# Kernel tuning notes

Measured on AMD Instinct MI355X. Metric: run time of the kernel, lower is better.

## Reference

```python
import jax, jax.numpy as jnp
import numpy as np

B, C, H, W = 4, 512, 48, 48
DQ = C // 8  # inter_rate = 8
N = H * W
EPS = 1e-5


def _local_mask(radius):
    r = np.arange(N) // W
    c = np.arange(N) % W
    d = np.maximum(np.abs(r[:, None] - r[None, :]), np.abs(c[:, None] - c[None, :]))
    return jnp.asarray(d <= radius)


def setup_inputs() -> dict:
    key = jax.random.key(0)
    ks = jax.random.split(key, 12)
    def nrm(k, shape, scale=0.04):
        return jax.random.normal(k, shape, dtype=jnp.float32) * scale
    zc = jnp.zeros((C,), jnp.float32)
    oc = jnp.ones((C,), jnp.float32)
    return {
        "x": jax.random.normal(ks[0], (B, C, H, W), dtype=jnp.float32),
        "Wq": nrm(ks[1], (DQ, C)), "bq": jnp.zeros((DQ,), jnp.float32),
        "Wk": nrm(ks[2], (DQ, C)), "bk": jnp.zeros((DQ,), jnp.float32),
        "Wv": nrm(ks[3], (C, C)), "bv": zc,
        "conv1_w": nrm(ks[4], (C, C, 3, 3)),
        "bn1_w": oc, "bn1_b": zc, "bn1_m": zc, "bn1_v": oc,
        "conv2_w": nrm(ks[5], (C, C, 3, 3)),
        "bn2_w": oc, "bn2_b": zc, "bn2_m": zc, "bn2_v": oc,
        "sig1_w": nrm(ks[6], (C, C)), "sig1_b": zc,
        "sig2_w": nrm(ks[7], (C, C)), "sig2_b": zc,
        "gamma": jnp.full((1,), 0.5, jnp.float32),
        "gamma1": jnp.full((1,), 0.3, jnp.float32),
        "gamma2": jnp.full((1,), 0.2, jnp.float32),
        "mask1": _local_mask(6),
        "mask2": _local_mask(12),
    }


def _masked_softmax(e, mask):
    # exp(e)*mask / sum(exp(e)*mask) == softmax with -inf outside mask
    e = e - jnp.max(e, axis=-1, keepdims=True)
    w = jnp.exp(e) * mask.astype(e.dtype)
    return w / jnp.sum(w, axis=-1, keepdims=True)


def _conv1x1(t, w, b):
    return jnp.einsum('bchw,dc->bdhw', t, w) + b[None, :, None, None]


def _conv3x3_bn_relu(t, w, g, beta, mu, var):
    y = jax.lax.conv_general_dilated(t, w, (1, 1), 'SAME',
                                     dimension_numbers=('NCHW', 'OIHW', 'NCHW'))
    scale = (g / jnp.sqrt(var + EPS))[None, :, None, None]
    y = (y - mu[None, :, None, None]) * scale + beta[None, :, None, None]
    return jax.nn.relu(y)


def _forward(x, Wq, bq, Wk, bk, Wv, bv, conv1_w, bn1_w, bn1_b, bn1_m, bn1_v,
             conv2_w, bn2_w, bn2_b, bn2_m, bn2_v, sig1_w, sig1_b, sig2_w, sig2_b,
             gamma, gamma1, gamma2, mask1, mask2):
    b, c, h, w = x.shape
    n = h * w
    q = _conv1x1(x, Wq, bq).reshape(b, -1, n)   # [B, d, N]
    k = _conv1x1(x, Wk, bk).reshape(b, -1, n)   # [B, d, N]
    energy = jnp.einsum('bdn,bdm->bnm', q, k)   # [B, N, N] (query rows)
    a0 = jax.nn.softmax(energy, axis=-1)
    a1 = _masked_softmax(energy, mask1)
    a2 = _masked_softmax(energy, mask2)
    v = _conv1x1(x, Wv, bv).reshape(b, c, n)
    # torch: bmm(value, attention.permute(0,2,1)) -> out[b,c,m] = sum_n v[b,c,n]*a[m,n]
    out0 = jnp.einsum('bcn,bmn->bcm', v, a0).reshape(b, c, h, w)
    out0 = gamma * out0 + x
    out0 = _conv3x3_bn_relu(out0, conv1_w, bn1_w, bn1_b, bn1_m, bn1_v)
    s1 = (jax.nn.sigmoid(_conv1x1(out0, sig1_w, sig1_b)) * out0).reshape(b, c, n)
    out1 = jnp.einsum('bcn,bmn->bcm', s1, a1).reshape(b, c, h, w)
    out1 = gamma1 * out1 + out0
    out1 = _conv3x3_bn_relu(out1, conv2_w, bn2_w, bn2_b, bn2_m, bn2_v)
    s2 = (jax.nn.sigmoid(_conv1x1(out1, sig2_w, sig2_b)) * out1).reshape(b, c, n)
    out2 = jnp.einsum('bcn,bmn->bcm', s2, a2).reshape(b, c, h, w)
    return gamma2 * out2 + out1


def reference(x, Wq, bq, Wk, bk, Wv, bv, conv1_w, bn1_w, bn1_b, bn1_m, bn1_v,
              conv2_w, bn2_w, bn2_b, bn2_m, bn2_v, sig1_w, sig1_b, sig2_w, sig2_b,
              gamma, gamma1, gamma2, mask1, mask2):
    return _forward(x, Wq, bq, Wk, bk, Wv, bv, conv1_w, bn1_w, bn1_b, bn1_m, bn1_v,
                    conv2_w, bn2_w, bn2_b, bn2_m, bn2_v, sig1_w, sig1_b, sig2_w, sig2_b,
                    gamma, gamma1, gamma2, mask1, mask2)
```

## Files before the change

kernel.cpp:

```cpp
#include <hip/hip_runtime.h>
#include <math.h>

#define BB 4
#define CC 512
#define HH 48
#define WW 48
#define NN 2304
#define DDQ 64
#define LDSP 72
#define PW 50
#define PROWS 2500

typedef __attribute__((ext_vector_type(4))) float f32x4;
typedef __attribute__((ext_vector_type(8))) _Float16 half8;
typedef __attribute__((ext_vector_type(4))) _Float16 half4;
typedef __attribute__((ext_vector_type(8))) short bf16x8;

__device__ __forceinline__ int imax(int a, int b) { return a > b ? a : b; }
__device__ __forceinline__ int imin(int a, int b) { return a < b ? a : b; }
__device__ __forceinline__ int prow(int m) {
    int h = m / WW, w = m - h * WW;
    return (h + 1) * PW + (w + 1);
}
__device__ __forceinline__ unsigned short f2bf(float f) {
    unsigned u = __float_as_uint(f);
    u += 0x7fffu + ((u >> 16) & 1u);
    return (unsigned short)(u >> 16);
}
__device__ __forceinline__ float bf2f(unsigned short s) {
    unsigned u = ((unsigned)s) << 16;
    return __uint_as_float(u);
}

typedef __attribute__((address_space(1))) unsigned int g_u32;
typedef __attribute__((address_space(3))) unsigned int l_u32;
__device__ __forceinline__ void gl16(const void* g, void* l) {
    __builtin_amdgcn_global_load_lds((const g_u32*)g, (l_u32*)l, 16, 0, 0);
}

#define BWAVE_IDX()                                  \
    int tid = threadIdx.x;                           \
    int wave = tid >> 6, lane = tid & 63;            \
    int wm = (wave >> 1) * 64, wn = (wave & 1) * 32; \
    int x = lane & 15, qq = lane >> 4;

__device__ __forceinline__ half8 fragld(const _Float16* T, int r, int c) {
    int kb = c ^ (r & 7);
    return *(const half8*)(T + r * 64 + kb * 8);
}
__device__ __forceinline__ bf16x8 fragld_b(const unsigned short* T, int r, int c) {
    int kb = c ^ (r & 7);
    return *(const bf16x8*)(T + r * 64 + kb * 8);
}

__device__ __forceinline__ void btile(const _Float16* As, const _Float16* Bs,
                                      f32x4 acc[4][2], int wm, int wn, int x, int qq) {
#pragma unroll
    for (int ks = 0; ks < 2; ++ks) {
        int c = ks * 4 + qq;
        half8 a0 = fragld(As, wm + x, c);
        half8 a1 = fragld(As, wm + 16 + x, c);
        half8 a2 = fragld(As, wm + 32 + x, c);
        half8 a3 = fragld(As, wm + 48 + x, c);
        half8 b0 = fragld(Bs, wn + x, c);
        half8 b1 = fragld(Bs, wn + 16 + x, c);
        acc[0][0] = __builtin_amdgcn_mfma_f32_16x16x32_f16(a0, b0, acc[0][0], 0, 0, 0);
        acc[0][1] = __builtin_amdgcn_mfma_f32_16x16x32_f16(a0, b1, acc[0][1], 0, 0, 0);
        acc[1][0] = __builtin_amdgcn_mfma_f32_16x16x32_f16(a1, b0, acc[1][0], 0, 0, 0);
        acc[1][1] = __builtin_amdgcn_mfma_f32_16x16x32_f16(a1, b1, acc[1][1], 0, 0, 0);
        acc[2][0] = __builtin_amdgcn_mfma_f32_16x16x32_f16(a2, b0, acc[2][0], 0, 0, 0);
        acc[2][1] = __builtin_amdgcn_mfma_f32_16x16x32_f16(a2, b1, acc[2][1], 0, 0, 0);
        acc[3][0] = __builtin_amdgcn_mfma_f32_16x16x32_f16(a3, b0, acc[3][0], 0, 0, 0);
        acc[3][1] = __builtin_amdgcn_mfma_f32_16x16x32_f16(a3, b1, acc[3][1], 0, 0, 0);
    }
}
__device__ __forceinline__ void btile_b(const unsigned short* As, const unsigned short* Bs,
                                        f32x4 acc[4][2], int wm, int wn, int x, int qq) {
#pragma unroll
    for (int ks = 0; ks < 2; ++ks) {
        int c = ks * 4 + qq;
        bf16x8 a0 = fragld_b(As, wm + x, c);
        bf16x8 a1 = fragld_b(As, wm + 16 + x, c);
        bf16x8 a2 = fragld_b(As, wm + 32 + x, c);
        bf16x8 a3 = fragld_b(As, wm + 48 + x, c);
        bf16x8 b0 = fragld_b(Bs, wn + x, c);
        bf16x8 b1 = fragld_b(Bs, wn + 16 + x, c);
        acc[0][0] = __builtin_amdgcn_mfma_f32_16x16x32_bf16(a0, b0, acc[0][0], 0, 0, 0);
        acc[0][1] = __builtin_amdgcn_mfma_f32_16x16x32_bf16(a0, b1, acc[0][1], 0, 0, 0);
        acc[1][0] = __builtin_amdgcn_mfma_f32_16x16x32_bf16(a1, b0, acc[1][0], 0, 0, 0);
        acc[1][1] = __builtin_amdgcn_mfma_f32_16x16x32_bf16(a1, b1, acc[1][1], 0, 0, 0);
        acc[2][0] = __builtin_amdgcn_mfma_f32_16x16x32_bf16(a2, b0, acc[2][0], 0, 0, 0);
        acc[2][1] = __builtin_amdgcn_mfma_f32_16x16x32_bf16(a2, b1, acc[2][1], 0, 0, 0);
        acc[3][0] = __builtin_amdgcn_mfma_f32_16x16x32_bf16(a3, b0, acc[3][0], 0, 0, 0);
        acc[3][1] = __builtin_amdgcn_mfma_f32_16x16x32_bf16(a3, b1, acc[3][1], 0, 0, 0);
    }
}

#define BACC_INIT()                                         \
    f32x4 zf = {0.f, 0.f, 0.f, 0.f};                        \
    f32x4 acc[4][2];                                        \
    _Pragma("unroll") for (int i_ = 0; i_ < 4; ++i_) {      \
        acc[i_][0] = zf; acc[i_][1] = zf; }

#define SLOT_A(i) int sb = (wave * 4 + (i)) * 64; int s = sb + lane; \
                  int r = s >> 3, kb = s & 7; int koff = ((kb ^ (r & 7)) << 3);
#define SLOT_B(i) int sb = (wave * 2 + (i)) * 64; int s = sb + lane; \
                  int r = s >> 3, kb = s & 7; int koff = ((kb ^ (r & 7)) << 3);

__device__ __forceinline__ void stage_rows(_Float16* dst, const _Float16* __restrict__ src,
                                           int ld, int row0, int k0, int tid) {
#pragma unroll
    for (int i = 0; i < 2; ++i) {
        int s = tid * 2 + i;
        int r = s >> 3, off = (s & 7) << 3;
        *(half8*)(dst + r * LDSP + off) =
            *(const half8*)(src + (size_t)(row0 + r) * ld + k0 + off);
    }
}
__device__ __forceinline__ void mfma_tile(const _Float16* As, const _Float16* Bs,
                                          f32x4 acc[2][2], int wm, int wn, int x, int qq) {
#pragma unroll
    for (int ks = 0; ks < 2; ++ks) {
        int kof = ks * 32 + qq * 8;
        half8 a0 = *(const half8*)(As + (wm + x) * LDSP + kof);
        half8 a1 = *(const half8*)(As + (wm + 16 + x) * LDSP + kof);
        half8 b0 = *(const half8*)(Bs + (wn + x) * LDSP + kof);
        half8 b1 = *(const half8*)(Bs + (wn + 16 + x) * LDSP + kof);
        acc[0][0] = __builtin_amdgcn_mfma_f32_16x16x32_f16(a0, b0, acc[0][0], 0, 0, 0);
        acc[0][1] = __builtin_amdgcn_mfma_f32_16x16x32_f16(a0, b1, acc[0][1], 0, 0, 0);
        acc[1][0] = __builtin_amdgcn_mfma_f32_16x16x32_f16(a1, b0, acc[1][0], 0, 0, 0);
        acc[1][1] = __builtin_amdgcn_mfma_f32_16x16x32_f16(a1, b1, acc[1][1], 0, 0, 0);
    }
}
#define WAVE_IDX()                             \
    int tid = threadIdx.x;                     \
    int wave = tid >> 6, lane = tid & 63;      \
    int wm = (wave >> 1) * 32, wn = (wave & 1) * 32; \
    int x = lane & 15, qq = lane >> 4;
#define ACC_INIT()                             \
    f32x4 zf = {0.f, 0.f, 0.f, 0.f};           \
    f32x4 acc[2][2];                           \
    acc[0][0] = zf; acc[0][1] = zf; acc[1][0] = zf; acc[1][1] = zf;

__global__ __launch_bounds__(256) void k_cast_multi(const float* __restrict__ s0,
                                                    const float* __restrict__ s1,
                                                    const float* __restrict__ s2,
                                                    _Float16* __restrict__ d0,
                                                    _Float16* __restrict__ d1,
                                                    _Float16* __restrict__ d2, int n) {
    const float* s = blockIdx.y == 0 ? s0 : (blockIdx.y == 1 ? s1 : s2);
    _Float16* d = blockIdx.y == 0 ? d0 : (blockIdx.y == 1 ? d1 : d2);
    for (int i = blockIdx.x * 256 + threadIdx.x; i < n; i += gridDim.x * 256)
        d[i] = (_Float16)s[i];
}

__global__ __launch_bounds__(256) void k_repack_conv2(const float* __restrict__ w1,
                                                      const float* __restrict__ w2,
                                                      _Float16* __restrict__ d1,
                                                      _Float16* __restrict__ d2) {
    const float* w = blockIdx.y ? w2 : w1;
    _Float16* dst = blockIdx.y ? d2 : d1;
    int i = blockIdx.x * 256 + threadIdx.x;
    if (i >= 9 * CC * CC) return;
    int r = i / (CC * CC);
    int rem = i - r * CC * CC;
    int co = rem / CC, ci = rem - (rem / CC) * CC;
    dst[i] = (_Float16)w[((size_t)co * CC + ci) * 9 + r];
}

__global__ __launch_bounds__(256) void k_transpose_x(const float* __restrict__ x,
                                                     _Float16* __restrict__ xT) {
    __shared__ float tile[32][33];
    int b = blockIdx.z;
    int c0 = blockIdx.y * 32, n0 = blockIdx.x * 32;
    int tx = threadIdx.x & 31, ty = threadIdx.x >> 5;
    const float* xb = x + (size_t)b * CC * NN;
#pragma unroll
    for (int rr = 0; rr < 32; rr += 8)
        tile[ty + rr][tx] = xb[(size_t)(c0 + ty + rr) * NN + n0 + tx];
    __syncthreads();
    _Float16* xTb = xT + (size_t)b * NN * CC;
#pragma unroll
    for (int rr = 0; rr < 32; rr += 8)
        xTb[(size_t)(n0 + ty + rr) * CC + c0 + tx] = (_Float16)tile[tx][ty + rr];
}

__global__ __launch_bounds__(256) void k_qkproj(const _Float16* __restrict__ Wq,
                                                const _Float16* __restrict__ Wk,
                                                const float* __restrict__ bq,
                                                const float* __restrict__ bk,
                                                const _Float16* __restrict__ xT,
                                                _Float16* __restrict__ qT,
                                                _Float16* __restrict__ kT) {
    __shared__ _Float16 As[64 * LDSP];
    __shared__ _Float16 Bs[64 * LDSP];
    WAVE_IDX();
    int j0 = blockIdx.x * 64, b = blockIdx.z;
    const _Float16* Wp = blockIdx.y ? Wk : Wq;
    const float* bias = blockIdx.y ? bk : bq;
    _Float16* outT = blockIdx.y ? kT : qT;
    const _Float16* xTb = xT + (size_t)b * NN * CC;
    ACC_INIT();
    for (int kc = 0; kc < CC; kc += 64) {
        stage_rows(As, Wp, CC, 0, kc, tid);
        stage_rows(Bs, xTb, CC, j0, kc, tid);
        __syncthreads();
        mfma_tile(As, Bs, acc, wm, wn, x, qq);
        __syncthreads();
    }
#pragma unroll
    for (int ms = 0; ms < 2; ++ms) {
        int R0 = wm + ms * 16 + qq * 4;
#pragma unroll
        for (int ns = 0; ns < 2; ++ns) {
            int Ccol = j0 + wn + ns * 16 + x;
            half4 t;
            t.x = (_Float16)(acc[ms][ns][0] + bias[R0 + 0]);
            t.y = (_Float16)(acc[ms][ns][1] + bias[R0 + 1]);
            t.z = (_Float16)(acc[ms][ns][2] + bias[R0 + 2]);
            t.w = (_Float16)(acc[ms][ns][3] + bias[R0 + 3]);
            *(half4*)(outT + ((size_t)b * NN + Ccol) * DDQ + R0) = t;
        }
    }
}

template <int EPI, int PAD>
__global__ __launch_bounds__(256) void k_cgemm(const _Float16* __restrict__ W,
                                               const float* __restrict__ bias,
                                               const _Float16* __restrict__ Bsrc,
                                               const float* __restrict__ gate,
                                               unsigned short* __restrict__ out) {
    __shared__ __align__(16) _Float16 As[2][128 * 64];
    __shared__ __align__(16) _Float16 Bs[2][64 * 64];
    BWAVE_IDX();
    int j0 = blockIdx.x * 64, i0 = blockIdx.y * 128, b = blockIdx.z;
    const _Float16* Bb = Bsrc + (size_t)b * (PAD ? (size_t)PROWS * CC : (size_t)NN * CC);

    const _Float16* aSrc[4]; int aOf[4];
#pragma unroll
    for (int i = 0; i < 4; ++i) {
        SLOT_A(i);
        aSrc[i] = W + (size_t)(i0 + r) * CC + koff;
        aOf[i] = sb * 8;
    }
    const _Float16* bSrc[2]; int bOf[2];
#pragma unroll
    for (int i = 0; i < 2; ++i) {
        SLOT_B(i);
        int row = PAD ? prow(j0 + r) : (j0 + r);
        bSrc[i] = Bb + (size_t)row * CC + koff;
        bOf[i] = sb * 8;
    }
    BACC_INIT();
#pragma unroll
    for (int i = 0; i < 4; ++i) gl16(aSrc[i], As[0] + aOf[i]);
#pragma unroll
    for (int i = 0; i < 2; ++i) gl16(bSrc[i], Bs[0] + bOf[i]);
    const int NSTEP = CC / 64;
#pragma unroll
    for (int t = 0; t < NSTEP - 1; ++t) {
        __syncthreads();
        int kc = (t + 1) << 6;
        int nb = (t + 1) & 1;
#pragma unroll
        for (int i = 0; i < 4; ++i) gl16(aSrc[i] + kc, As[nb] + aOf[i]);
#pragma unroll
        for (int i = 0; i < 2; ++i) gl16(bSrc[i] + kc, Bs[nb] + bOf[i]);
        btile(As[t & 1], Bs[t & 1], acc, wm, wn, x, qq);
    }
    __syncthreads();
    btile(As[(NSTEP - 1) & 1], Bs[(NSTEP - 1) & 1], acc, wm, wn, x, qq);
#pragma unroll
    for (int mt = 0; mt < 4; ++mt) {
        int R0 = i0 + wm + mt * 16 + qq * 4;
#pragma unroll
        for (int nt = 0; nt < 2; ++nt) {
            int Ccol = j0 + wn + nt * 16 + x;
#pragma unroll
            for (int e = 0; e < 4; ++e) {
                float v = acc[mt][nt][e] + bias[R0 + e];
                size_t idx = ((size_t)b * CC + R0 + e) * NN + Ccol;
                if (EPI == 1) v = gate[idx] / (1.f + __expf(-v));
                out[idx] = f2bf(v);
            }
        }
    }
}

__global__ __launch_bounds__(256) void k_exp(const _Float16* __restrict__ qT,
                                             const _Float16* __restrict__ kT,
                                             unsigned short* __restrict__ attnB,
                                             float* __restrict__ rowsum, int rad) {
    __shared__ _Float16 qs[64 * LDSP];
    __shared__ _Float16 ks[64 * LDSP];
    __shared__ unsigned short Eh[64 * 72];
    __shared__ float psum[512];
    WAVE_IDX();
    int j0 = blockIdx.x * 64, i0 = blockIdx.y * 64, b = blockIdx.z;
    if (rad > 0) {
        int hlo = i0 / WW, hhi = (i0 + 63) / WW;
        int h2lo = imax(0, hlo - rad), h2hi = imin(HH - 1, hhi + rad);
        int klo = (h2lo * WW) & ~63;
        int khi = imin(NN, ((h2hi + 1) * WW + 63) & ~63);
        if (j0 + 64 <= klo || j0 >= khi) return;
    }
    stage_rows(qs, qT + (size_t)b * NN * DDQ, DDQ, i0, 0, tid);
    stage_rows(ks, kT + (size_t)b * NN * DDQ, DDQ, j0, 0, tid);
    __syncthreads();
    ACC_INIT();
    mfma_tile(qs, ks, acc, wm, wn, x, qq);
#pragma unroll
    for (int ns = 0; ns < 2; ++ns) {
        int col = wn + ns * 16 + x;
        int gn = j0 + col;
        int hn = gn / WW, cn = gn % WW;
#pragma unroll
        for (int ms = 0; ms < 2; ++ms)
#pragma unroll
            for (int e = 0; e < 4; ++e) {
                int row = wm + ms * 16 + qq * 4 + e;
                int gm = i0 + row;
                bool valid = true;
                if (rad > 0) {
                    int dh = gm / WW - hn; if (dh < 0) dh = -dh;
                    int dc = gm % WW - cn; if (dc < 0) dc = -dc;
                    valid = (dh <= rad) && (dc <= rad);
                }
                float w = valid ? __expf(acc[ms][ns][e]) : 0.f;
                Eh[row * 72 + col] = f2bf(w);
            }
    }
    __syncthreads();
#pragma unroll
    for (int t = 0; t < 2; ++t) {
        int s = tid + t * 256;
        int r = s >> 3, cg = (s & 7) << 3;
        bf16x8 v = *(const bf16x8*)(Eh + r * 72 + cg);
        *(bf16x8*)(attnB + ((size_t)b * NN + i0 + r) * NN + j0 + cg) = v;
        float ss = 0.f;
#pragma unroll
        for (int j = 0; j < 8; ++j) ss += bf2f((unsigned short)v[j]);
        psum[s] = ss;
    }
    __syncthreads();
    if (tid < 64) {
        float tot = 0.f;
#pragma unroll
        for (int g = 0; g < 8; ++g) tot += psum[tid * 8 + g];
        atomicAdd(rowsum + (size_t)b * NN + i0 + tid, tot);
    }
}

__global__ __launch_bounds__(256) void k_attn(const unsigned short* __restrict__ A,
                                              const unsigned short* __restrict__ attnB,
                                              const float* __restrict__ rowsum,
                                              const float* __restrict__ res,
                                              const float* __restrict__ gamma,
                                              float* __restrict__ outF,
                                              _Float16* __restrict__ outT, int rad) {
    __shared__ __align__(16) unsigned short As[2][128 * 64];
    __shared__ __align__(16) unsigned short Bs[2][64 * 64];
    BWAVE_IDX();
    int j0 = blockIdx.x * 64, i0 = blockIdx.y * 128, b = blockIdx.z;
    int klo = 0, khi = NN;
    if (rad > 0) {
        int hlo = j0 / WW, hhi = (j0 + 63) / WW;
        int h2lo = imax(0, hlo - rad), h2hi = imin(HH - 1, hhi + rad);
        klo = (h2lo * WW) & ~63;
        khi = imin(NN, ((h2hi + 1) * WW + 63) & ~63);
    }
    const unsigned short* Ab = A + (size_t)b * CC * NN;
    const unsigned short* Tb = attnB + (size_t)b * NN * NN;

    const unsigned short* aSrc[4]; int aOf[4];
#pragma unroll
    for (int i = 0; i < 4; ++i) {
        SLOT_A(i);
        aSrc[i] = Ab + (size_t)(i0 + r) * NN + koff + klo;
        aOf[i] = sb * 8;
    }
    const unsigned short* bSrc[2]; int bOf[2];
#pragma unroll
    for (int i = 0; i < 2; ++i) {
        SLOT_B(i);
        bSrc[i] = Tb + (size_t)(j0 + r) * NN + koff + klo;
        bOf[i] = sb * 8;
    }
    BACC_INIT();
    int nsteps = (khi - klo) >> 6;
#pragma unroll
    for (int i = 0; i < 4; ++i) gl16(aSrc[i], As[0] + aOf[i]);
#pragma unroll
    for (int i = 0; i < 2; ++i) gl16(bSrc[i], Bs[0] + bOf[i]);
    for (int t = 0; t < nsteps - 1; ++t) {
        __syncthreads();
        int kc = (t + 1) << 6;
        int nb = (t + 1) & 1;
#pragma unroll
        for (int i = 0; i < 4; ++i) gl16(aSrc[i] + kc, As[nb] + aOf[i]);
#pragma unroll
        for (int i = 0; i < 2; ++i) gl16(bSrc[i] + kc, Bs[nb] + bOf[i]);
        btile_b(As[t & 1], Bs[t & 1], acc, wm, wn, x, qq);
    }
    __syncthreads();
    btile_b(As[(nsteps - 1) & 1], Bs[(nsteps - 1) & 1], acc, wm, wn, x, qq);
    float g = gamma[0];
#pragma unroll
    for (int mt = 0; mt < 4; ++mt) {
        int R0 = i0 + wm + mt * 16 + qq * 4;
#pragma unroll
        for (int nt = 0; nt < 2; ++nt) {
            int Ccol = j0 + wn + nt * 16 + x;
            float linv = g / fmaxf(rowsum[(size_t)b * NN + Ccol], 1e-30f);
            float v[4];
#pragma unroll
            for (int e = 0; e < 4; ++e)
                v[e] = acc[mt][nt][e] * linv + res[((size_t)b * CC + R0 + e) * NN + Ccol];
            if (outT) {
                half4 t;
                t.x = (_Float16)v[0]; t.y = (_Float16)v[1];
                t.z = (_Float16)v[2]; t.w = (_Float16)v[3];
                *(half4*)(outT + ((size_t)b * PROWS + prow(Ccol)) * CC + R0) = t;
            }
            if (outF) {
#pragma unroll
                for (int e = 0; e < 4; ++e)
                    outF[((size_t)b * CC + R0 + e) * NN + Ccol] = v[e];
            }
        }
    }
}

__global__ __launch_bounds__(256) void k_conv3(const _Float16* __restrict__ Arep,
                                               const _Float16* __restrict__ Tpad,
                                               const float* __restrict__ bng,
                                               const float* __restrict__ bnb,
                                               const float* __restrict__ bnm,
                                               const float* __restrict__ bnv,
                                               float* __restrict__ outF,
                                               _Float16* __restrict__ outT) {
    __shared__ __align__(16) _Float16 As[2][128 * 64];
    __shared__ __align__(16) _Float16 Bs[2][64 * 64];
    BWAVE_IDX();
    int j0 = blockIdx.x * 64, i0 = blockIdx.y * 128, b = blockIdx.z;
    const _Float16* Tb = Tpad + (size_t)b * PROWS * CC;

    const _Float16* aBase[4]; int aOf[4];
#pragma unroll
    for (int i = 0; i < 4; ++i) {
        SLOT_A(i);
        aBase[i] = Arep + (size_t)(i0 + r) * CC + koff;
        aOf[i] = sb * 8;
    }
    const _Float16* bBase[2]; int bOf[2];
#pragma unroll
    for (int i = 0; i < 2; ++i) {
        SLOT_B(i);
        bBase[i] = Tb + (size_t)prow(j0 + r) * CC + koff;
        bOf[i] = sb * 8;
    }
    BACC_INIT();

#define STAGE_CONV(u, nb)                                                       \
    {                                                                           \
        const int rt_ = (u) >> 3, ci_ = ((u) & 7) << 6;                         \
        const int r3_ = rt_ / 3;                                                \
        const ptrdiff_t aoff_ = (ptrdiff_t)rt_ * CC * CC + ci_;                 \
        const ptrdiff_t boff_ =                                                 \
            (ptrdiff_t)((r3_ - 1) * PW + (rt_ - r3_ * 3 - 1)) * CC + ci_;       \
        _Pragma("unroll") for (int i = 0; i < 4; ++i)                           \
            gl16(aBase[i] + aoff_, As[nb] + aOf[i]);                            \
        _Pragma("unroll") for (int i = 0; i < 2; ++i)                           \
            gl16(bBase[i] + boff_, Bs[nb] + bOf[i]);                            \
    }

    STAGE_CONV(0, 0);
    const int TOT = 9 * (CC / 64);
#pragma unroll
    for (int t = 0; t < TOT - 1; ++t) {
        __syncthreads();
        STAGE_CONV(t + 1, (t + 1) & 1);
        btile(As[t & 1], Bs[t & 1], acc, wm, wn, x, qq);
    }
    __syncthreads();
    btile(As[(TOT - 1) & 1], Bs[(TOT - 1) & 1], acc, wm, wn, x, qq);
#undef STAGE_CONV

#pragma unroll
    for (int mt = 0; mt < 4; ++mt) {
        int R0 = i0 + wm + mt * 16 + qq * 4;
        float sc[4], sh[4];
#pragma unroll
        for (int e = 0; e < 4; ++e) {
            sc[e] = bng[R0 + e] * rsqrtf(bnv[R0 + e] + 1e-5f);
            sh[e] = bnb[R0 + e] - bnm[R0 + e] * sc[e];
        }
#pragma unroll
        for (int nt = 0; nt < 2; ++nt) {
            int Ccol = j0 + wn + nt * 16 + x;
            float v[4];
#pragma unroll
            for (int e = 0; e < 4; ++e) {
                float t = acc[mt][nt][e] * sc[e] + sh[e];
                v[e] = t > 0.f ? t : 0.f;
                outF[((size_t)b * CC + R0 + e) * NN + Ccol] = v[e];
            }
            half4 t4;
            t4.x = (_Float16)v[0]; t4.y = (_Float16)v[1];
            t4.z = (_Float16)v[2]; t4.w = (_Float16)v[3];
            *(half4*)(outT + ((size_t)b * PROWS + prow(Ccol)) * CC + R0) = t4;
        }
    }
}

extern "C" void kernel_launch(void* const* d_in, const int* in_sizes, int n_in,
                              void* d_out, int out_size, void* d_ws, size_t ws_size,
                              hipStream_t stream) {
    const float* xin  = (const float*)d_in[0];
    const float* Wq   = (const float*)d_in[1];
    const float* bq   = (const float*)d_in[2];
    const float* Wk   = (const float*)d_in[3];
    const float* bk   = (const float*)d_in[4];
    const float* Wv   = (const float*)d_in[5];
    const float* bv   = (const float*)d_in[6];
    const float* c1w  = (const float*)d_in[7];
    const float* bn1w = (const float*)d_in[8];
    const float* bn1b = (const float*)d_in[9];
    const float* bn1m = (const float*)d_in[10];
    const float* bn1v = (const float*)d_in[11];
    const float* c2w  = (const float*)d_in[12];
    const float* bn2w = (const float*)d_in[13];
    const float* bn2b = (const float*)d_in[14];
    const float* bn2m = (const float*)d_in[15];
    const float* bn2v = (const float*)d_in[16];
    const float* s1w  = (const float*)d_in[17];
    const float* s1b  = (const float*)d_in[18];
    const float* s2w  = (const float*)d_in[19];
    const float* s2b  = (const float*)d_in[20];
    const float* gamma  = (const float*)d_in[21];
    const float* gamma1 = (const float*)d_in[22];
    const float* gamma2 = (const float*)d_in[23];

    float* out = (float*)d_out;

    char* p = (char*)d_ws;
    unsigned short* attn = (unsigned short*)p; p += (size_t)BB * NN * NN * 2;
    _Float16* xT    = (_Float16*)p; p += (size_t)BB * NN * CC * 2;
    _Float16* qT    = (_Float16*)p; p += (size_t)BB * NN * DDQ * 2;
    _Float16* kT    = (_Float16*)p; p += (size_t)BB * NN * DDQ * 2;
    unsigned short* vsB = (unsigned short*)p; p += (size_t)BB * CC * NN * 2;
    _Float16* TattnP= (_Float16*)p; p += (size_t)BB * PROWS * CC * 2;
    _Float16* TconvP= (_Float16*)p; p += (size_t)BB * PROWS * CC * 2;
    float*    rR    = (float*)p;    p += (size_t)BB * CC * NN * 4;
    _Float16* wq_h  = (_Float16*)p; p += (size_t)DDQ * CC * 2;
    _Float16* wk_h  = (_Float16*)p; p += (size_t)DDQ * CC * 2;
    _Float16* wv_h  = (_Float16*)p; p += (size_t)CC * CC * 2;
    _Float16* s1_h  = (_Float16*)p; p += (size_t)CC * CC * 2;
    _Float16* s2_h  = (_Float16*)p; p += (size_t)CC * CC * 2;
    _Float16* crep1 = (_Float16*)p; p += (size_t)9 * CC * CC * 2;
    _Float16* crep2 = (_Float16*)p; p += (size_t)9 * CC * CC * 2;
    float*    rowsum= (float*)p;    p += (size_t)3 * BB * NN * 4;

    dim3 blk(256);

    hipMemsetAsync(TattnP, 0, (size_t)BB * PROWS * CC * 2, stream);
    hipMemsetAsync(TconvP, 0, (size_t)BB * PROWS * CC * 2, stream);
    hipMemsetAsync(rowsum, 0, (size_t)3 * BB * NN * 4, stream);

    k_cast_multi<<<dim3(128, 2), blk, 0, stream>>>(Wq, Wk, nullptr, wq_h, wk_h, nullptr, DDQ * CC);
    k_cast_multi<<<dim3(1024, 3), blk, 0, stream>>>(Wv, s1w, s2w, wv_h, s1_h, s2_h, CC * CC);
    k_repack_conv2<<<dim3((9 * CC * CC + 255) / 256, 2), blk, 0, stream>>>(c1w, c2w, crep1, crep2);
    k_transpose_x<<<dim3(NN / 32, CC / 32, BB), blk, 0, stream>>>(xin, xT);

    dim3 gQK(NN / 64, 2, BB);
    dim3 gExp(NN / 64, NN / 64, BB);
    dim3 gBig(NN / 64, CC / 128, BB);

    float* rs0 = rowsum;
    float* rs1 = rowsum + (size_t)BB * NN;
    float* rs2 = rowsum + (size_t)2 * BB * NN;

    k_qkproj<<<gQK, blk, 0, stream>>>(wq_h, wk_h, bq, bk, xT, qT, kT);
    k_cgemm<0, 0><<<gBig, blk, 0, stream>>>(wv_h, bv, xT, nullptr, vsB);

    k_exp<<<gExp, blk, 0, stream>>>(qT, kT, attn, rs0, -1);
    k_attn<<<gBig, blk, 0, stream>>>(vsB, attn, rs0, xin, gamma, nullptr, TattnP, -1);
    k_conv3<<<gBig, blk, 0, stream>>>(crep1, TattnP, bn1w, bn1b, bn1m, bn1v, rR, TconvP);

    k_cgemm<1, 1><<<gBig, blk, 0, stream>>>(s1_h, s1b, TconvP, rR, vsB);
    k_exp<<<gExp, blk, 0, stream>>>(qT, kT, attn, rs1, 6);
    k_attn<<<gBig, blk, 0, stream>>>(vsB, attn, rs1, rR, gamma1, nullptr, TattnP, 6);
    k_conv3<<<gBig, blk, 0, stream>>>(crep2, TattnP, bn2w, bn2b, bn2m, bn2v, rR, TconvP);

    k_cgemm<1, 1><<<gBig, blk, 0, stream>>>(s2_h, s2b, TconvP, rR, vsB);
    k_exp<<<gExp, blk, 0, stream>>>(qT, kT, attn, rs2, 12);
    k_attn<<<gBig, blk, 0, stream>>>(vsB, attn, rs2, rR, gamma2, out, nullptr, 12);
}
```

Before: 510.8 us.

## Keep two global-to-LDS stages in flight with explicit vmcnt waits

Three GEMM-style kernels (1x1 conv, attention matmul, 3x3 conv) change their double-buffered global_load_lds loop. Each now issues two stages up front and waits with s_waitcnt vmcnt(6) and raw barriers, so the next tile's loads stay outstanding while the current tile is computed. This replaces __syncthreads, which waits for all outstanding loads. It adds a second barrier per step so a buffer is not overwritten while other waves still read it. The 3x3 conv loop also drops full unrolling for unroll 2.

```diff
diff --git a/kernel.cpp b/kernel.cpp
--- a/kernel.cpp
+++ b/kernel.cpp
@@ -37,6 +37,10 @@
 __device__ __forceinline__ void gl16(const void* g, void* l) {
     __builtin_amdgcn_global_load_lds((const g_u32*)g, (l_u32*)l, 16, 0, 0);
 }
+
+#define WAIT6()  asm volatile("s_waitcnt vmcnt(6)" ::: "memory")
+#define WAIT0()  asm volatile("s_waitcnt vmcnt(0)" ::: "memory")
+#define BAR()    { __builtin_amdgcn_s_barrier(); asm volatile("" ::: "memory"); }
 
 #define BWAVE_IDX()                                  \
     int tid = threadIdx.x;                           \
@@ -252,24 +256,29 @@
         bOf[i] = sb * 8;
     }
     BACC_INIT();
-#pragma unroll
-    for (int i = 0; i < 4; ++i) gl16(aSrc[i], As[0] + aOf[i]);
-#pragma unroll
-    for (int i = 0; i < 2; ++i) gl16(bSrc[i], Bs[0] + bOf[i]);
+#define STG_G(kc, nb)                                                          \
+    { _Pragma("unroll") for (int i = 0; i < 4; ++i)                            \
+          gl16(aSrc[i] + (kc), As[nb] + aOf[i]);                               \
+      _Pragma("unroll") for (int i = 0; i < 2; ++i)                            \
+          gl16(bSrc[i] + (kc), Bs[nb] + bOf[i]); }
+    STG_G(0, 0);
+    STG_G(64, 1);
     const int NSTEP = CC / 64;
 #pragma unroll
-    for (int t = 0; t < NSTEP - 1; ++t) {
-        __syncthreads();
-        int kc = (t + 1) << 6;
-        int nb = (t + 1) & 1;
-#pragma unroll
-        for (int i = 0; i < 4; ++i) gl16(aSrc[i] + kc, As[nb] + aOf[i]);
-#pragma unroll
-        for (int i = 0; i < 2; ++i) gl16(bSrc[i] + kc, Bs[nb] + bOf[i]);
+    for (int t = 0; t + 2 < NSTEP; ++t) {
+        WAIT6();
+        BAR();
         btile(As[t & 1], Bs[t & 1], acc, wm, wn, x, qq);
-    }
-    __syncthreads();
+        BAR();
+        STG_G((t + 2) * 64, (t & 1));
+    }
+    WAIT6();
+    BAR();
+    btile(As[(NSTEP - 2) & 1], Bs[(NSTEP - 2) & 1], acc, wm, wn, x, qq);
+    WAIT0();
+    BAR();
     btile(As[(NSTEP - 1) & 1], Bs[(NSTEP - 1) & 1], acc, wm, wn, x, qq);
+#undef STG_G
 #pragma unroll
     for (int mt = 0; mt < 4; ++mt) {
         int R0 = i0 + wm + mt * 16 + qq * 4;
@@ -388,22 +397,27 @@
     }
     BACC_INIT();
     int nsteps = (khi - klo) >> 6;
-#pragma unroll
-    for (int i = 0; i < 4; ++i) gl16(aSrc[i], As[0] + aOf[i]);
-#pragma unroll
-    for (int i = 0; i < 2; ++i) gl16(bSrc[i], Bs[0] + bOf[i]);
-    for (int t = 0; t < nsteps - 1; ++t) {
-        __syncthreads();
-        int kc = (t + 1) << 6;
-        int nb = (t + 1) & 1;
-#pragma unroll
-        for (int i = 0; i < 4; ++i) gl16(aSrc[i] + kc, As[nb] + aOf[i]);
-#pragma unroll
-        for (int i = 0; i < 2; ++i) gl16(bSrc[i] + kc, Bs[nb] + bOf[i]);
+#define STG_T(kc, nb)                                                          \
+    { _Pragma("unroll") for (int i = 0; i < 4; ++i)                            \
+          gl16(aSrc[i] + (kc), As[nb] + aOf[i]);                               \
+      _Pragma("unroll") for (int i = 0; i < 2; ++i)                            \
+          gl16(bSrc[i] + (kc), Bs[nb] + bOf[i]); }
+    STG_T(0, 0);
+    STG_T(64, 1);
+    for (int t = 0; t + 2 < nsteps; ++t) {
+        WAIT6();
+        BAR();
         btile_b(As[t & 1], Bs[t & 1], acc, wm, wn, x, qq);
-    }
-    __syncthreads();
+        BAR();
+        STG_T((t + 2) << 6, (t & 1));
+    }
+    WAIT6();
+    BAR();
+    btile_b(As[(nsteps - 2) & 1], Bs[(nsteps - 2) & 1], acc, wm, wn, x, qq);
+    WAIT0();
+    BAR();
     btile_b(As[(nsteps - 1) & 1], Bs[(nsteps - 1) & 1], acc, wm, wn, x, qq);
+#undef STG_T
     float g = gamma[0];
 #pragma unroll
     for (int mt = 0; mt < 4; ++mt) {
@@ -463,10 +477,10 @@
 
 #define STAGE_CONV(u, nb)                                                       \
     {                                                                           \
-        const int rt_ = (u) >> 3, ci_ = ((u) & 7) << 6;                         \
-        const int r3_ = rt_ / 3;                                                \
-        const ptrdiff_t aoff_ = (ptrdiff_t)rt_ * CC * CC + ci_;                 \
-        const ptrdiff_t boff_ =                                                 \
+        int rt_ = (u) >> 3, ci_ = ((u) & 7) << 6;                               \
+        int r3_ = rt_ / 3;                                                      \
+        ptrdiff_t aoff_ = (ptrdiff_t)rt_ * (CC * CC) + ci_;                     \
+        ptrdiff_t boff_ =                                                       \
             (ptrdiff_t)((r3_ - 1) * PW + (rt_ - r3_ * 3 - 1)) * CC + ci_;       \
         _Pragma("unroll") for (int i = 0; i < 4; ++i)                           \
             gl16(aBase[i] + aoff_, As[nb] + aOf[i]);                            \
@@ -475,14 +489,21 @@
     }
 
     STAGE_CONV(0, 0);
+    STAGE_CONV(1, 1);
     const int TOT = 9 * (CC / 64);
-#pragma unroll
-    for (int t = 0; t < TOT - 1; ++t) {
-        __syncthreads();
-        STAGE_CONV(t + 1, (t + 1) & 1);
+#pragma unroll 2
+    for (int t = 0; t + 2 < TOT; ++t) {
+        WAIT6();
+        BAR();
         btile(As[t & 1], Bs[t & 1], acc, wm, wn, x, qq);
-    }
-    __syncthreads();
+        BAR();
+        STAGE_CONV(t + 2, (t & 1));
+    }
+    WAIT6();
+    BAR();
+    btile(As[(TOT - 2) & 1], Bs[(TOT - 2) & 1], acc, wm, wn, x, qq);
+    WAIT0();
+    BAR();
     btile(As[(TOT - 1) & 1], Bs[(TOT - 1) & 1], acc, wm, wn, x, qq);
 #undef STAGE_CONV
 
```

After: 488.3 us. 4.4% less time.
